# Kernel optimization log

Hardware: AMD Instinct MI355X
Metric: run time of the kernel (lower is better)

The kernel has to match this reference:

```python
import jax, jax.numpy as jnp
import numpy as np

NUM_NODES = 10000
NUM_EDGES = 640000
D_FEAT = 128

def setup_inputs() -> dict:
    key = jax.random.key(0)
    k1, k2 = jax.random.split(key)
    x = jax.random.normal(k1, (NUM_NODES, D_FEAT), dtype=jnp.float32)
    edge_index = jax.random.randint(k2, (2, NUM_EDGES), 0, NUM_NODES, dtype=jnp.int64)
    return {"x": x, "edge_index": edge_index}

def reference(x, edge_index):
    # MessagePassing(aggr='add') with default message/update:
    # msg = x[src]; out[n] = sum of msg over edges with dst == n
    src, dst = edge_index[0], edge_index[1]
    msg = x[src]                                   # [num_edges, d]
    out = jax.ops.segment_sum(msg, dst, num_segments=NUM_NODES)  # [num_nodes, d]
    return out
```

## Files before the change

kernel.cpp:

```cpp
#include <hip/hip_runtime.h>

#define NUM_NODES 10000
#define NUM_EDGES 640000
#define D_FEAT 128

#define BSHIFT 4
#define NPB 16
#define NB 625
#define BLOCKS 256
#define EPB (NUM_EDGES / BLOCKS)
#define CELL_CAP 32
#define MAXB 1344

#define XB_U4 (NUM_NODES * 16)
#define CVT_PER_BLOCK (XB_U4 / BLOCKS)


__device__ __forceinline__ unsigned bf16_rne(float f) {
    unsigned u = __float_as_uint(f);
    return (u + 0x7FFFu + ((u >> 16) & 1u)) >> 16;
}

__global__ __launch_bounds__(256) void scatter_cvt_kernel(
    const int* __restrict__ ei, const float4* __restrict__ x4,
    uint4* __restrict__ xb, unsigned* __restrict__ cnt,
    unsigned* __restrict__ slots) {
    __shared__ int cur[NB];
    int t = threadIdx.x, b = blockIdx.x;
    for (int i = t; i < NB; i += 256) cur[i] = 0;

    int cbase = b * CVT_PER_BLOCK;
    for (int i = t; i < CVT_PER_BLOCK; i += 256) {
        int o = cbase + i;
        float4 a = x4[2 * o];
        float4 c = x4[2 * o + 1];
        uint4 w;
        w.x = bf16_rne(a.x) | (bf16_rne(a.y) << 16);
        w.y = bf16_rne(a.z) | (bf16_rne(a.w) << 16);
        w.z = bf16_rne(c.x) | (bf16_rne(c.y) << 16);
        w.w = bf16_rne(c.z) | (bf16_rne(c.w) << 16);
        xb[o] = w;
    }
    __syncthreads();

    int base = b * EPB;
    for (int j = t; j < EPB; j += 256) {
        int src = ei[base + j];
        int dst = ei[NUM_EDGES + base + j];
        int k = dst >> BSHIFT;
        int pos = atomicAdd(&cur[k], 1);
        if (pos < CELL_CAP)
            slots[(unsigned)(k * BLOCKS + b) * CELL_CAP + (unsigned)pos] =
                ((unsigned)(dst & (NPB - 1)) << 16) | (unsigned)src;
    }
    __syncthreads();
    for (int i = t; i < NB; i += 256)
        cnt[b * NB + i] = (unsigned)min(cur[i], CELL_CAP);
}

__global__ __launch_bounds__(256) void sort_gather_kernel(
    const uint4* __restrict__ xb,
    const unsigned* __restrict__ cnt,
    const uint4* __restrict__ slots4,
    float4* __restrict__ out4)
{
    __shared__ int s_cnt[BLOCKS];
    __shared__ unsigned s_src[MAXB];
    __shared__ int h[NPB];
    __shared__ int off16[NPB];
    __shared__ int cur16[NPB];

    int k = blockIdx.x;
    int t = threadIdx.x;

    if (t < NPB) h[t] = 0;
    s_cnt[t] = (int)cnt[t * NB + k];
    __syncthreads();

    const uint4* sb = slots4 + (unsigned)k * BLOCKS * (CELL_CAP / 4);
    uint4 w4[8];
    int vc[8];
    #pragma unroll
    for (int i = 0; i < 8; ++i) {
        int c = (t >> 3) + 32 * i;
        int sub = t & 7;
        w4[i] = sb[c * 8 + sub];
        int v = s_cnt[c] - sub * 4;
        vc[i] = max(0, min(4, v));
        if (vc[i] > 0) atomicAdd(&h[w4[i].x >> 16], 1);
        if (vc[i] > 1) atomicAdd(&h[w4[i].y >> 16], 1);
        if (vc[i] > 2) atomicAdd(&h[w4[i].z >> 16], 1);
        if (vc[i] > 3) atomicAdd(&h[w4[i].w >> 16], 1);
    }
    __syncthreads();

    if (t == 0) {
        int run = 0;
        for (int m = 0; m < NPB; ++m) { off16[m] = run; cur16[m] = run; run += h[m]; }
    }
    __syncthreads();

    #pragma unroll
    for (int i = 0; i < 8; ++i) {
        if (vc[i] > 0) { int p = atomicAdd(&cur16[w4[i].x >> 16], 1); if (p < MAXB) s_src[p] = w4[i].x & 0xFFFFu; }
        if (vc[i] > 1) { int p = atomicAdd(&cur16[w4[i].y >> 16], 1); if (p < MAXB) s_src[p] = w4[i].y & 0xFFFFu; }
        if (vc[i] > 2) { int p = atomicAdd(&cur16[w4[i].z >> 16], 1); if (p < MAXB) s_src[p] = w4[i].z & 0xFFFFu; }
        if (vc[i] > 3) { int p = atomicAdd(&cur16[w4[i].w >> 16], 1); if (p < MAXB) s_src[p] = w4[i].w & 0xFFFFu; }
    }
    __syncthreads();

    int wave = t >> 6;
    int lane = t & 63;
    int q    = lane >> 4;
    int sub  = lane & 15;

    for (int m = wave; m < NPB; m += 4) {
        int node = k * NPB + m;
        int beg = off16[m];
        int ec  = h[m];
        float a0 = 0.f, a1 = 0.f, a2 = 0.f, a3 = 0.f;
        float a4 = 0.f, a5 = 0.f, a6 = 0.f, a7 = 0.f;
        int j = 0;
        for (; j + 4 <= ec; j += 4) {
            unsigned s = s_src[beg + j + q];
            uint4 w = xb[s * 16u + sub];
            a0 += __uint_as_float(w.x << 16);
            a1 += __uint_as_float(w.x & 0xFFFF0000u);
            a2 += __uint_as_float(w.y << 16);
            a3 += __uint_as_float(w.y & 0xFFFF0000u);
            a4 += __uint_as_float(w.z << 16);
            a5 += __uint_as_float(w.z & 0xFFFF0000u);
            a6 += __uint_as_float(w.w << 16);
            a7 += __uint_as_float(w.w & 0xFFFF0000u);
        }
        if (j + q < ec) {
            unsigned s = s_src[beg + j + q];
            uint4 w = xb[s * 16u + sub];
            a0 += __uint_as_float(w.x << 16);
            a1 += __uint_as_float(w.x & 0xFFFF0000u);
            a2 += __uint_as_float(w.y << 16);
            a3 += __uint_as_float(w.y & 0xFFFF0000u);
            a4 += __uint_as_float(w.z << 16);
            a5 += __uint_as_float(w.z & 0xFFFF0000u);
            a6 += __uint_as_float(w.w << 16);
            a7 += __uint_as_float(w.w & 0xFFFF0000u);
        }
        a0 += __shfl_down(a0, 32); a1 += __shfl_down(a1, 32);
        a2 += __shfl_down(a2, 32); a3 += __shfl_down(a3, 32);
        a4 += __shfl_down(a4, 32); a5 += __shfl_down(a5, 32);
        a6 += __shfl_down(a6, 32); a7 += __shfl_down(a7, 32);
        a0 += __shfl_down(a0, 16); a1 += __shfl_down(a1, 16);
        a2 += __shfl_down(a2, 16); a3 += __shfl_down(a3, 16);
        a4 += __shfl_down(a4, 16); a5 += __shfl_down(a5, 16);
        a6 += __shfl_down(a6, 16); a7 += __shfl_down(a7, 16);
        if (q == 0) {
            unsigned o = (unsigned)node * 32u + (unsigned)sub * 2u;
            out4[o]     = make_float4(a0, a1, a2, a3);
            out4[o + 1] = make_float4(a4, a5, a6, a7);
        }
    }
}

extern "C" void kernel_launch(void* const* d_in, const int* in_sizes, int n_in,
                              void* d_out, int out_size, void* d_ws, size_t ws_size,
                              hipStream_t stream) {
    const float* x   = (const float*)d_in[0];
    const int*   ei  = (const int*)d_in[1];
    float*       out = (float*)d_out;

    uint4*    xb    = (uint4*)d_ws;
    unsigned* cnt   = (unsigned*)(xb + XB_U4);
    unsigned* slots = cnt + BLOCKS * NB;

    scatter_cvt_kernel<<<BLOCKS, 256, 0, stream>>>(
        ei, (const float4*)x, xb, cnt, slots);

    sort_gather_kernel<<<NB, 256, 0, stream>>>(
        xb, cnt, (const uint4*)slots, (float4*)out);
}
```

Before: 91.08 us.

## Widen blocks, prefetch edges early, and software-pipeline two-node gather loop

Measured after the change: 85.01 us. 6.7% less time.

```diff
diff --git a/kernel.cpp b/kernel.cpp
--- a/kernel.cpp
+++ b/kernel.cpp
@@ -21,17 +21,16 @@
     return (u + 0x7FFFu + ((u >> 16) & 1u)) >> 16;
 }
 
-__global__ __launch_bounds__(256) void scatter_cvt_kernel(
+__global__ __launch_bounds__(1024) void scatter_cvt_kernel(
     const int* __restrict__ ei, const float4* __restrict__ x4,
     uint4* __restrict__ xb, unsigned* __restrict__ cnt,
     unsigned* __restrict__ slots) {
     __shared__ int cur[NB];
     int t = threadIdx.x, b = blockIdx.x;
-    for (int i = t; i < NB; i += 256) cur[i] = 0;
-
-    int cbase = b * CVT_PER_BLOCK;
-    for (int i = t; i < CVT_PER_BLOCK; i += 256) {
-        int o = cbase + i;
+    if (t < NB) cur[t] = 0;
+
+    if (t < CVT_PER_BLOCK) {
+        int o = b * CVT_PER_BLOCK + t;
         float4 a = x4[2 * o];
         float4 c = x4[2 * o + 1];
         uint4 w;
@@ -41,24 +40,71 @@
         w.w = bf16_rne(c.z) | (bf16_rne(c.w) << 16);
         xb[o] = w;
     }
-    __syncthreads();
 
     int base = b * EPB;
-    for (int j = t; j < EPB; j += 256) {
-        int src = ei[base + j];
-        int dst = ei[NUM_EDGES + base + j];
-        int k = dst >> BSHIFT;
+    int s0 = ei[base + t];
+    int d0 = ei[NUM_EDGES + base + t];
+    int s1 = ei[base + t + 1024];
+    int d1 = ei[NUM_EDGES + base + t + 1024];
+    int s2 = 0, d2 = 0;
+    bool has2 = (t + 2048) < EPB;
+    if (has2) {
+        s2 = ei[base + t + 2048];
+        d2 = ei[NUM_EDGES + base + t + 2048];
+    }
+    __syncthreads();
+
+    {
+        int k = d0 >> BSHIFT;
         int pos = atomicAdd(&cur[k], 1);
         if (pos < CELL_CAP)
             slots[(unsigned)(k * BLOCKS + b) * CELL_CAP + (unsigned)pos] =
-                ((unsigned)(dst & (NPB - 1)) << 16) | (unsigned)src;
-    }
-    __syncthreads();
-    for (int i = t; i < NB; i += 256)
-        cnt[b * NB + i] = (unsigned)min(cur[i], CELL_CAP);
-}
-
-__global__ __launch_bounds__(256) void sort_gather_kernel(
+                ((unsigned)(d0 & (NPB - 1)) << 16) | (unsigned)s0;
+    }
+    {
+        int k = d1 >> BSHIFT;
+        int pos = atomicAdd(&cur[k], 1);
+        if (pos < CELL_CAP)
+            slots[(unsigned)(k * BLOCKS + b) * CELL_CAP + (unsigned)pos] =
+                ((unsigned)(d1 & (NPB - 1)) << 16) | (unsigned)s1;
+    }
+    if (has2) {
+        int k = d2 >> BSHIFT;
+        int pos = atomicAdd(&cur[k], 1);
+        if (pos < CELL_CAP)
+            slots[(unsigned)(k * BLOCKS + b) * CELL_CAP + (unsigned)pos] =
+                ((unsigned)(d2 & (NPB - 1)) << 16) | (unsigned)s2;
+    }
+    __syncthreads();
+    if (t < NB) cnt[b * NB + t] = (unsigned)min(cur[t], CELL_CAP);
+}
+
+__device__ __forceinline__ void acc8(float* a, uint4 w) {
+    a[0] += __uint_as_float(w.x << 16);
+    a[1] += __uint_as_float(w.x & 0xFFFF0000u);
+    a[2] += __uint_as_float(w.y << 16);
+    a[3] += __uint_as_float(w.y & 0xFFFF0000u);
+    a[4] += __uint_as_float(w.z << 16);
+    a[5] += __uint_as_float(w.z & 0xFFFF0000u);
+    a[6] += __uint_as_float(w.w << 16);
+    a[7] += __uint_as_float(w.w & 0xFFFF0000u);
+}
+
+__device__ __forceinline__ void reduce_write(float* a, int node, int q, int sub,
+                                             float4* __restrict__ out4) {
+    #pragma unroll
+    for (int r = 0; r < 8; ++r) {
+        a[r] += __shfl_down(a[r], 32);
+        a[r] += __shfl_down(a[r], 16);
+    }
+    if (q == 0) {
+        unsigned o = (unsigned)node * 32u + (unsigned)sub * 2u;
+        out4[o]     = make_float4(a[0], a[1], a[2], a[3]);
+        out4[o + 1] = make_float4(a[4], a[5], a[6], a[7]);
+    }
+}
+
+__global__ __launch_bounds__(512) void sort_gather_kernel(
     const uint4* __restrict__ xb,
     const unsigned* __restrict__ cnt,
     const uint4* __restrict__ slots4,
@@ -74,17 +120,17 @@
     int t = threadIdx.x;
 
     if (t < NPB) h[t] = 0;
-    s_cnt[t] = (int)cnt[t * NB + k];
+    if (t < BLOCKS) s_cnt[t] = (int)cnt[t * NB + k];
     __syncthreads();
 
     const uint4* sb = slots4 + (unsigned)k * BLOCKS * (CELL_CAP / 4);
-    uint4 w4[8];
-    int vc[8];
+    uint4 w4[4];
+    int vc[4];
     #pragma unroll
-    for (int i = 0; i < 8; ++i) {
-        int c = (t >> 3) + 32 * i;
+    for (int i = 0; i < 4; ++i) {
+        int c = (t >> 3) + 64 * i;
         int sub = t & 7;
-        w4[i] = sb[c * 8 + sub];
+        w4[i] = sb[t + 512 * i];
         int v = s_cnt[c] - sub * 4;
         vc[i] = max(0, min(4, v));
         if (vc[i] > 0) atomicAdd(&h[w4[i].x >> 16], 1);
@@ -94,14 +140,21 @@
     }
     __syncthreads();
 
-    if (t == 0) {
-        int run = 0;
-        for (int m = 0; m < NPB; ++m) { off16[m] = run; cur16[m] = run; run += h[m]; }
+    if (t < NPB) {
+        int v = h[t];
+        int s = v;
+        #pragma unroll
+        for (int d = 1; d < 16; d <<= 1) {
+            int u = __shfl_up(s, d, 16);
+            if (t >= d) s += u;
+        }
+        off16[t] = s - v;
+        cur16[t] = s - v;
     }
     __syncthreads();
 
     #pragma unroll
-    for (int i = 0; i < 8; ++i) {
+    for (int i = 0; i < 4; ++i) {
         if (vc[i] > 0) { int p = atomicAdd(&cur16[w4[i].x >> 16], 1); if (p < MAXB) s_src[p] = w4[i].x & 0xFFFFu; }
         if (vc[i] > 1) { int p = atomicAdd(&cur16[w4[i].y >> 16], 1); if (p < MAXB) s_src[p] = w4[i].y & 0xFFFFu; }
         if (vc[i] > 2) { int p = atomicAdd(&cur16[w4[i].z >> 16], 1); if (p < MAXB) s_src[p] = w4[i].z & 0xFFFFu; }
@@ -114,51 +167,39 @@
     int q    = lane >> 4;
     int sub  = lane & 15;
 
-    for (int m = wave; m < NPB; m += 4) {
-        int node = k * NPB + m;
-        int beg = off16[m];
-        int ec  = h[m];
-        float a0 = 0.f, a1 = 0.f, a2 = 0.f, a3 = 0.f;
-        float a4 = 0.f, a5 = 0.f, a6 = 0.f, a7 = 0.f;
-        int j = 0;
-        for (; j + 4 <= ec; j += 4) {
-            unsigned s = s_src[beg + j + q];
-            uint4 w = xb[s * 16u + sub];
-            a0 += __uint_as_float(w.x << 16);
-            a1 += __uint_as_float(w.x & 0xFFFF0000u);
-            a2 += __uint_as_float(w.y << 16);
-            a3 += __uint_as_float(w.y & 0xFFFF0000u);
-            a4 += __uint_as_float(w.z << 16);
-            a5 += __uint_as_float(w.z & 0xFFFF0000u);
-            a6 += __uint_as_float(w.w << 16);
-            a7 += __uint_as_float(w.w & 0xFFFF0000u);
-        }
-        if (j + q < ec) {
-            unsigned s = s_src[beg + j + q];
-            uint4 w = xb[s * 16u + sub];
-            a0 += __uint_as_float(w.x << 16);
-            a1 += __uint_as_float(w.x & 0xFFFF0000u);
-            a2 += __uint_as_float(w.y << 16);
-            a3 += __uint_as_float(w.y & 0xFFFF0000u);
-            a4 += __uint_as_float(w.z << 16);
-            a5 += __uint_as_float(w.z & 0xFFFF0000u);
-            a6 += __uint_as_float(w.w << 16);
-            a7 += __uint_as_float(w.w & 0xFFFF0000u);
-        }
-        a0 += __shfl_down(a0, 32); a1 += __shfl_down(a1, 32);
-        a2 += __shfl_down(a2, 32); a3 += __shfl_down(a3, 32);
-        a4 += __shfl_down(a4, 32); a5 += __shfl_down(a5, 32);
-        a6 += __shfl_down(a6, 32); a7 += __shfl_down(a7, 32);
-        a0 += __shfl_down(a0, 16); a1 += __shfl_down(a1, 16);
-        a2 += __shfl_down(a2, 16); a3 += __shfl_down(a3, 16);
-        a4 += __shfl_down(a4, 16); a5 += __shfl_down(a5, 16);
-        a6 += __shfl_down(a6, 16); a7 += __shfl_down(a7, 16);
-        if (q == 0) {
-            unsigned o = (unsigned)node * 32u + (unsigned)sub * 2u;
-            out4[o]     = make_float4(a0, a1, a2, a3);
-            out4[o + 1] = make_float4(a4, a5, a6, a7);
-        }
-    }
+    int mA = wave;
+    int mB = wave + 8;
+    int begA = off16[mA], ecA = h[mA];
+    int begB = off16[mB], ecB = h[mB];
+    int lastA = ecA > 0 ? ecA - 1 : 0;
+    int lastB = ecB > 0 ? ecB - 1 : 0;
+
+    float aA[8] = {0.f, 0.f, 0.f, 0.f, 0.f, 0.f, 0.f, 0.f};
+    float aB[8] = {0.f, 0.f, 0.f, 0.f, 0.f, 0.f, 0.f, 0.f};
+
+    bool vA = q < ecA, vB = q < ecB;
+    unsigned iA = (unsigned)min(begA + min(q, lastA), MAXB - 1);
+    unsigned iB = (unsigned)min(begB + min(q, lastB), MAXB - 1);
+    uint4 wA = xb[(s_src[iA] & 0xFFFFu) * 16u + (unsigned)sub];
+    uint4 wB = xb[(s_src[iB] & 0xFFFFu) * 16u + (unsigned)sub];
+
+    int jmax = max(ecA, ecB);
+    for (int j = 0; j < jmax; j += 4) {
+        int jn = j + 4;
+        unsigned iA2 = (unsigned)min(begA + min(jn + q, lastA), MAXB - 1);
+        unsigned iB2 = (unsigned)min(begB + min(jn + q, lastB), MAXB - 1);
+        uint4 wA2 = xb[(s_src[iA2] & 0xFFFFu) * 16u + (unsigned)sub];
+        uint4 wB2 = xb[(s_src[iB2] & 0xFFFFu) * 16u + (unsigned)sub];
+        bool vA2 = (jn + q) < ecA;
+        bool vB2 = (jn + q) < ecB;
+        if (vA) acc8(aA, wA);
+        if (vB) acc8(aB, wB);
+        wA = wA2; vA = vA2;
+        wB = wB2; vB = vB2;
+    }
+
+    reduce_write(aA, k * NPB + mA, q, sub, out4);
+    reduce_write(aB, k * NPB + mB, q, sub, out4);
 }
 
 extern "C" void kernel_launch(void* const* d_in, const int* in_sizes, int n_in,
@@ -172,9 +213,9 @@
     unsigned* cnt   = (unsigned*)(xb + XB_U4);
     unsigned* slots = cnt + BLOCKS * NB;
 
-    scatter_cvt_kernel<<<BLOCKS, 256, 0, stream>>>(
+    scatter_cvt_kernel<<<BLOCKS, 1024, 0, stream>>>(
         ei, (const float4*)x, xb, cnt, slots);
 
-    sort_gather_kernel<<<NB, 256, 0, stream>>>(
+    sort_gather_kernel<<<NB, 512, 0, stream>>>(
         xb, cnt, (const uint4*)slots, (float4*)out);
 }
```
